# Performance work log

Measured on AMD Instinct MI355X. Metric: run time of the kernel, lower is better.

Reference implementation:

```python
import jax, jax.numpy as jnp
import numpy as np

DOWNSAMPLING_K = 64  # number of pooled key/value positions


def setup_inputs() -> dict:
    key = jax.random.key(0)
    ks = jax.random.split(key, 8)
    B, S, H, N, D = 4, 4096, 1024, 16, 64
    s_in = 0.02  # glorot-like scale for H=1024 fan-in
    return {
        "query": jax.random.normal(ks[0], (B, S, H), jnp.float32),
        "key": jax.random.normal(ks[1], (B, S, H), jnp.float32),
        "value": jax.random.normal(ks[2], (B, S, H), jnp.float32),
        "Wq": jax.random.normal(ks[3], (H, N, D), jnp.float32) * s_in,
        "bq": jnp.zeros((N, D), jnp.float32),
        "Wk": jax.random.normal(ks[4], (H, N, D), jnp.float32) * s_in,
        "bk": jnp.zeros((N, D), jnp.float32),
        "Wv": jax.random.normal(ks[5], (H, N, D), jnp.float32) * s_in,
        "bv": jnp.zeros((N, D), jnp.float32),
        "Wo": jax.random.normal(ks[6], (N, D, H), jnp.float32) * s_in,
        "bo": jnp.zeros((H,), jnp.float32),
        "step": 0,
        "train": 0,
    }


def _downsample(x, k):
    # x: [B, S, N, D] -> mean-pool along sequence into k buckets -> [B, k, N, D]
    B, S, N, D = x.shape
    return x.reshape(B, k, S // k, N, D).mean(axis=2)


def reference(query, key, value, Wq, bq, Wk, bk, Wv, bv, Wo, bo, step, train):
    # QKV projections (DenseGeneral features=(num_heads, head_dim))
    q = jnp.einsum("bsh,hnd->bsnd", query, Wq) + bq  # [B,S,N,D]
    k = jnp.einsum("bsh,hnd->bsnd", key, Wk) + bk
    v = jnp.einsum("bsh,hnd->bsnd", value, Wv) + bv
    # Downsampled (sparse) attention: pool K,V to DOWNSAMPLING_K positions
    kd = _downsample(k, DOWNSAMPLING_K)  # [B,K,N,D]
    vd = _downsample(v, DOWNSAMPLING_K)
    scale = 1.0 / jnp.sqrt(jnp.asarray(q.shape[-1], q.dtype))
    scores = jnp.einsum("bsnd,bknd->bnsk", q, kd) * scale  # [B,N,S,K]
    attn = jax.nn.softmax(scores, axis=-1)
    a_v = jnp.einsum("bnsk,bknd->bsnd", attn, vd)  # [B,S,N,D]
    # Output projection (DenseGeneral over (-2,-1))
    out = jnp.einsum("bsnd,ndh->bsh", a_v, Wo) + bo  # [B,S,H]
    return out
```

## Files before the change

kernel.cpp:

```cpp
#include <hip/hip_runtime.h>

typedef unsigned short u16;
typedef unsigned int u32;
typedef __attribute__((ext_vector_type(8))) short bf16x8_t;
typedef __attribute__((ext_vector_type(4))) float f32x4_t;


#define MFMA_BF16 __builtin_amdgcn_mfma_f32_16x16x32_bf16

__device__ __forceinline__ u16 f2bf(float f) {
  union { float f; u32 u; } a; a.f = f;
  u32 u = a.u;
  u32 r = (u + 0x7FFFu + ((u >> 16) & 1u)) >> 16;
  return (u16)r;
}

__device__ __forceinline__ void async_load16(const void* g, void* l) {
  __builtin_amdgcn_global_load_lds(
      (const __attribute__((address_space(1))) void*)g,
      (__attribute__((address_space(3))) void*)l, 16, 0, 0);
}

__device__ __forceinline__ void stage64(const u16* __restrict__ src,
                                        char* lds_base, int t) {
  const int r = t >> 3;
  const int gch = (t & 7) ^ (r & 7);
  async_load16(src + (size_t)r * 1024 + gch * 8, lds_base + (t >> 6) * 1024);
}

__global__ __launch_bounds__(512) void fused_stream(
    const float* __restrict__ query, const float* __restrict__ key,
    const float* __restrict__ value, const float* __restrict__ W0,
    const float* __restrict__ W1, const float* __restrict__ W2,
    const float* __restrict__ W3, u16* __restrict__ qcvt, u16* __restrict__ keyd,
    u16* __restrict__ valued, u16* __restrict__ T0, u16* __restrict__ T1,
    u16* __restrict__ T2, u16* __restrict__ T3) {
  __shared__ char smem[32768];
  const int z = blockIdx.x;
  const int t = threadIdx.x;
  if (z < 512) {
    f32x4_t (*part)[256] = (f32x4_t(*)[256])smem;
    const int bkk = z & 255;
    const float* x = (z >= 256) ? value : key;
    u16* xd = (z >= 256) ? valued : keyd;
    const int lane = t & 63, w = t >> 6;
    const float* base = x + (size_t)bkk * 65536 + (size_t)w * 8 * 1024;
#define LD4(j, s) \
  __builtin_nontemporal_load((const f32x4_t*)(base + (size_t)(j) * 1024 + ((s) * 64 + lane) * 4))
    f32x4_t a0 = {0.f, 0.f, 0.f, 0.f}, a1 = a0, a2 = a0, a3 = a0;
    f32x4_t u0 = LD4(0, 0), u1 = LD4(0, 1), u2 = LD4(0, 2), u3 = LD4(0, 3);
    f32x4_t u4 = LD4(1, 0), u5 = LD4(1, 1), u6 = LD4(1, 2), u7 = LD4(1, 3);
    f32x4_t v0 = LD4(2, 0), v1 = LD4(2, 1), v2 = LD4(2, 2), v3 = LD4(2, 3);
    f32x4_t v4 = LD4(3, 0), v5 = LD4(3, 1), v6 = LD4(3, 2), v7 = LD4(3, 3);
    a0 += u0; a1 += u1; a2 += u2; a3 += u3;
    a0 += u4; a1 += u5; a2 += u6; a3 += u7;
    u0 = LD4(4, 0); u1 = LD4(4, 1); u2 = LD4(4, 2); u3 = LD4(4, 3);
    u4 = LD4(5, 0); u5 = LD4(5, 1); u6 = LD4(5, 2); u7 = LD4(5, 3);
    a0 += v0; a1 += v1; a2 += v2; a3 += v3;
    a0 += v4; a1 += v5; a2 += v6; a3 += v7;
    v0 = LD4(6, 0); v1 = LD4(6, 1); v2 = LD4(6, 2); v3 = LD4(6, 3);
    v4 = LD4(7, 0); v5 = LD4(7, 1); v6 = LD4(7, 2); v7 = LD4(7, 3);
    a0 += u0; a1 += u1; a2 += u2; a3 += u3;
    a0 += u4; a1 += u5; a2 += u6; a3 += u7;
    a0 += v0; a1 += v1; a2 += v2; a3 += v3;
    a0 += v4; a1 += v5; a2 += v6; a3 += v7;
#undef LD4
    part[w][0 * 64 + lane] = a0;
    part[w][1 * 64 + lane] = a1;
    part[w][2 * 64 + lane] = a2;
    part[w][3 * 64 + lane] = a3;
    __syncthreads();
    if (t < 256) {
      f32x4_t s = {0.f, 0.f, 0.f, 0.f};
#pragma unroll
      for (int w2 = 0; w2 < 8; ++w2) s += part[w2][t];
      ushort4 r;
      r.x = f2bf(s[0] * 0.015625f);
      r.y = f2bf(s[1] * 0.015625f);
      r.z = f2bf(s[2] * 0.015625f);
      r.w = f2bf(s[3] * 0.015625f);
      *(ushort4*)(xd + (size_t)bkk * 1024 + t * 4) = r;
    }
  } else if (z < 4608) {
    const size_t i = ((size_t)(z - 512) * 512 + t) * 8;
    const f32x4_t a = __builtin_nontemporal_load((const f32x4_t*)(query + i));
    const f32x4_t b = __builtin_nontemporal_load((const f32x4_t*)(query + i + 4));
    bf16x8_t o;
    o[0] = (short)f2bf(a[0]); o[1] = (short)f2bf(a[1]);
    o[2] = (short)f2bf(a[2]); o[3] = (short)f2bf(a[3]);
    o[4] = (short)f2bf(b[0]); o[5] = (short)f2bf(b[1]);
    o[6] = (short)f2bf(b[2]); o[7] = (short)f2bf(b[3]);
    *(bf16x8_t*)(qcvt + i) = o;
  } else {
    float (*tile)[65] = (float(*)[65])smem;
    const int blk = z - 4608;
    const int wsel = blk >> 8, tidx = blk & 255;
    const float* W = (wsel == 0) ? W0 : (wsel == 1) ? W1 : (wsel == 2) ? W2 : W3;
    u16* WT = (wsel == 0) ? T0 : (wsel == 1) ? T1 : (wsel == 2) ? T2 : T3;
    const int tr = (tidx >> 4) * 64;
    const int tc = (tidx & 15) * 64;
#pragma unroll
    for (int i = 0; i < 8; ++i) {
      int idx = i * 512 + t;
      int r = idx >> 6, c = idx & 63;
      tile[r][c] = __builtin_nontemporal_load(W + (size_t)(tr + r) * 1024 + tc + c);
    }
    __syncthreads();
#pragma unroll
    for (int i = 0; i < 8; ++i) {
      int idx = i * 512 + t;
      int r = idx >> 6, c = idx & 63;
      WT[(size_t)(tc + r) * 1024 + tr + c] = f2bf(tile[c][r]);
    }
  }
}

__global__ __launch_bounds__(256) void gemm_kv(const u16* __restrict__ A0,
                                               const u16* __restrict__ A1,
                                               const u16* __restrict__ BT0,
                                               const u16* __restrict__ BT1,
                                               const float* __restrict__ bias0,
                                               const float* __restrict__ bias1,
                                               u16* __restrict__ C0,
                                               u16* __restrict__ C1) {
  constexpr int K = 1024, BK = 32;
  __shared__ u16 sA[128 * BK];
  __shared__ u16 sB[128 * BK];
  const int z = blockIdx.z;
  const u16* A = z ? A1 : A0;
  const u16* BT = z ? BT1 : BT0;
  const float* bias = z ? bias1 : bias0;
  u16* Cv = z ? C1 : C0;
  const int t = threadIdx.x;
  const int lane = t & 63;
  const int w = t >> 6;
  const int wr = w >> 1, wc = w & 1;
  const int m0 = blockIdx.x * 128;
  const int n0 = blockIdx.y * 128;
  const int c16 = lane & 15, r16 = lane >> 4;

  f32x4_t acc[4][4] = {};

  for (int k0 = 0; k0 < K; k0 += BK) {
#pragma unroll
    for (int i = 0; i < 2; ++i) {
      const int idx = i * 256 + t;
      const int row = idx >> 2, ch = idx & 3;
      const int gch = ch ^ ((row >> 1) & 3);
      async_load16(A + (size_t)(m0 + row) * K + k0 + gch * 8,
                   (char*)sA + (i * 256 + w * 64) * 16);
    }
#pragma unroll
    for (int i = 0; i < 2; ++i) {
      const int idx = i * 256 + t;
      const int row = idx >> 2, ch = idx & 3;
      const int gch = ch ^ ((row >> 1) & 3);
      async_load16(BT + (size_t)(n0 + row) * K + k0 + gch * 8,
                   (char*)sB + (i * 256 + w * 64) * 16);
    }
    __syncthreads();

    bf16x8_t af[4], bfv[4];
#pragma unroll
    for (int m = 0; m < 4; ++m) {
      const int ra = wr * 64 + m * 16 + c16;
      af[m] = *(const bf16x8_t*)&sA[ra * BK + ((r16 ^ ((ra >> 1) & 3)) << 3)];
    }
#pragma unroll
    for (int n = 0; n < 4; ++n) {
      const int rb = wc * 64 + n * 16 + c16;
      bfv[n] = *(const bf16x8_t*)&sB[rb * BK + ((r16 ^ ((rb >> 1) & 3)) << 3)];
    }
#pragma unroll
    for (int m = 0; m < 4; ++m)
#pragma unroll
      for (int n = 0; n < 4; ++n)
        acc[m][n] = MFMA_BF16(af[m], bfv[n], acc[m][n], 0, 0, 0);
    __syncthreads();
  }

#pragma unroll
  for (int m = 0; m < 4; ++m) {
    const int row0 = m0 + wr * 64 + m * 16 + r16 * 4;
#pragma unroll
    for (int n = 0; n < 4; ++n) {
      const int col = n0 + wc * 64 + n * 16 + c16;
      const float bvl = bias[col];
#pragma unroll
      for (int i = 0; i < 4; ++i) {
        const float val = acc[m][n][i] + bvl;
        if (z)
          Cv[(size_t)col * 256 + row0 + i] = f2bf(val);
        else
          Cv[(size_t)(row0 + i) * 1024 + col] = f2bf(val);
      }
    }
  }
}

#define GEMM256_KLOOP(A_, BT_)                                                          \
  const u16* Ab = (A_) + (size_t)bx * 256 * 1024;                                       \
  const u16* Bb = (BT_) + (size_t)by * 256 * 1024;                                      \
  stage64(Ab,                   lds,                 t);                                \
  stage64(Ab + 128 * 1024,      lds + 128 * 128,     t);                                \
  stage64(Bb,                   lds + 32768,         t);                                \
  stage64(Bb + 64 * 1024,       lds + 32768 + 8192,  t);                                \
  stage64(Bb + 128 * 1024,      lds + 32768 + 16384, t);                                \
  stage64(Bb + 192 * 1024,      lds + 32768 + 24576, t);                                \
  stage64(Ab + 64 * 1024,       lds + 64 * 128,      t);                                \
  stage64(Ab + 192 * 1024,      lds + 192 * 128,     t);                                \
  stage64(Ab + 64,              lds + 65536,         t);                                \
  stage64(Ab + 128 * 1024 + 64, lds + 65536 + 16384, t);                                \
  stage64(Bb + 64,              lds + 98304,         t);                                \
  stage64(Bb + 64 * 1024 + 64,  lds + 98304 + 8192,  t);                                \
  stage64(Bb + 128 * 1024 + 64, lds + 98304 + 16384, t);                                \
  stage64(Bb + 192 * 1024 + 64, lds + 98304 + 24576, t);                                \
  asm volatile("s_waitcnt vmcnt(6)" ::: "memory");                                      \
  __builtin_amdgcn_s_barrier();                                                         \
  for (int kt = 0; kt < 16; ++kt) {                                                     \
    const int slot = kt & 1;                                                            \
    const u16* sAs = (const u16*)(lds + slot * 65536);                                  \
    const u16* sBs = (const u16*)(lds + slot * 65536 + 32768);                          \
    char* sAn = lds + (slot ^ 1) * 65536;                                               \
    char* sAc = lds + slot * 65536;                                                     \
    char* sBc = lds + slot * 65536 + 32768;                                             \
    const int k1 = (kt < 15 ? kt + 1 : 15) * 64;                                        \
    const int k2 = (kt < 14 ? kt + 2 : 15) * 64;                                        \
    bf16x8_t af[4][2];                                                                  \
    _Pragma("unroll") for (int m = 0; m < 4; ++m) {                                     \
      const int row = wm * 128 + m * 16 + c16;                                          \
      _Pragma("unroll") for (int kk = 0; kk < 2; ++kk)                                  \
        af[m][kk] = *(const bf16x8_t*)&sAs[row * 64 + (((kk * 4 + r16) ^ c7) << 3)];    \
    }                                                                                   \
    _Pragma("unroll") for (int n = 0; n < 2; ++n) {                                     \
      const int row = wn * 64 + n * 16 + c16;                                           \
      _Pragma("unroll") for (int kk = 0; kk < 2; ++kk)                                  \
        bfr[n][kk] = *(const bf16x8_t*)&sBs[row * 64 + (((kk * 4 + r16) ^ c7) << 3)];   \
    }                                                                                   \
    stage64(Ab + (size_t)64 * 1024 + k1,  sAn + 64 * 128,  t);                          \
    stage64(Ab + (size_t)192 * 1024 + k1, sAn + 192 * 128, t);                          \
    asm volatile("" ::: "memory");                                                      \
    __builtin_amdgcn_s_barrier();                                                       \
    asm volatile("s_waitcnt lgkmcnt(0)" ::: "memory");                                  \
    __builtin_amdgcn_sched_barrier(0);                                                  \
    __builtin_amdgcn_s_setprio(1);                                                      \
    _Pragma("unroll") for (int m = 0; m < 4; ++m)                                       \
      _Pragma("unroll") for (int n = 0; n < 2; ++n)                                     \
        _Pragma("unroll") for (int kk = 0; kk < 2; ++kk)                                \
          acc[m][n] = MFMA_BF16(af[m][kk], bfr[n][kk], acc[m][n], 0, 0, 0);             \
    __builtin_amdgcn_s_setprio(0);                                                      \
    asm volatile("" ::: "memory");                                                      \
    __builtin_amdgcn_s_barrier();                                                       \
    _Pragma("unroll") for (int n = 2; n < 4; ++n) {                                     \
      const int row = wn * 64 + n * 16 + c16;                                           \
      _Pragma("unroll") for (int kk = 0; kk < 2; ++kk)                                  \
        bfr[n][kk] = *(const bf16x8_t*)&sBs[row * 64 + (((kk * 4 + r16) ^ c7) << 3)];   \
    }                                                                                   \
    stage64(Ab + k2,                      sAc,             t);                          \
    stage64(Ab + (size_t)128 * 1024 + k2, sAc + 128 * 128, t);                          \
    asm volatile("" ::: "memory");                                                      \
    __builtin_amdgcn_s_barrier();                                                       \
    asm volatile("s_waitcnt lgkmcnt(0)" ::: "memory");                                  \
    __builtin_amdgcn_sched_barrier(0);                                                  \
    __builtin_amdgcn_s_setprio(1);                                                      \
    _Pragma("unroll") for (int m = 0; m < 4; ++m)                                       \
      _Pragma("unroll") for (int n = 2; n < 4; ++n)                                     \
        _Pragma("unroll") for (int kk = 0; kk < 2; ++kk)                                \
          acc[m][n] = MFMA_BF16(af[m][kk], bfr[n][kk], acc[m][n], 0, 0, 0);             \
    __builtin_amdgcn_s_setprio(0);                                                      \
    asm volatile("s_waitcnt vmcnt(10)" ::: "memory");                                   \
    __builtin_amdgcn_s_barrier();                                                       \
    _Pragma("unroll") for (int m = 0; m < 4; ++m) {                                     \
      const int row = wm * 128 + 64 + m * 16 + c16;                                     \
      _Pragma("unroll") for (int kk = 0; kk < 2; ++kk)                                  \
        af[m][kk] = *(const bf16x8_t*)&sAs[row * 64 + (((kk * 4 + r16) ^ c7) << 3)];    \
    }                                                                                   \
    stage64(Bb + k2,                     sBc,        t);                                \
    stage64(Bb + (size_t)64 * 1024 + k2, sBc + 8192, t);                                \
    asm volatile("" ::: "memory");                                                      \
    __builtin_amdgcn_s_barrier();                                                       \
    asm volatile("s_waitcnt lgkmcnt(0)" ::: "memory");                                  \
    __builtin_amdgcn_sched_barrier(0);                                                  \
    __builtin_amdgcn_s_setprio(1);                                                      \
    _Pragma("unroll") for (int m = 0; m < 4; ++m)                                       \
      _Pragma("unroll") for (int n = 0; n < 2; ++n)                                     \
        _Pragma("unroll") for (int kk = 0; kk < 2; ++kk)                                \
          acc[4 + m][n] = MFMA_BF16(af[m][kk], bfr[n][kk], acc[4 + m][n], 0, 0, 0);     \
    __builtin_amdgcn_s_setprio(0);                                                      \
    asm volatile("" ::: "memory");                                                      \
    __builtin_amdgcn_s_barrier();                                                       \
    stage64(Bb + (size_t)128 * 1024 + k2, sBc + 16384, t);                              \
    stage64(Bb + (size_t)192 * 1024 + k2, sBc + 24576, t);                              \
    asm volatile("" ::: "memory");                                                      \
    __builtin_amdgcn_s_barrier();                                                       \
    __builtin_amdgcn_sched_barrier(0);                                                  \
    __builtin_amdgcn_s_setprio(1);                                                      \
    _Pragma("unroll") for (int m = 0; m < 4; ++m)                                       \
      _Pragma("unroll") for (int n = 2; n < 4; ++n)                                     \
        _Pragma("unroll") for (int kk = 0; kk < 2; ++kk)                                \
          acc[4 + m][n] = MFMA_BF16(af[m][kk], bfr[n][kk], acc[4 + m][n], 0, 0, 0);     \
    __builtin_amdgcn_s_setprio(0);                                                      \
    asm volatile("s_waitcnt vmcnt(8)" ::: "memory");                                    \
    __builtin_amdgcn_s_barrier();                                                       \
  }

template <bool C_BF16>
__global__ __launch_bounds__(512) void gemm256(const u16* __restrict__ A,
                                               const u16* __restrict__ BT,
                                               const float* __restrict__ bias,
                                               void* __restrict__ Cv) {
  __shared__ u16 sAB[65536];
  char* lds = (char*)sAB;
  const int t = threadIdx.x;
  const int lane = t & 63;
  const int w = t >> 6;
  const int wm = w >> 2, wn = w & 3;
  const int c16 = lane & 15, r16 = lane >> 4, c7 = c16 & 7;
  const int tile = (blockIdx.x & 7) * 32 + (blockIdx.x >> 3);
  const int bx = tile >> 2, by = tile & 3;
  f32x4_t acc[8][4] = {};
  bf16x8_t bfr[4][2];
  GEMM256_KLOOP(A, BT)
#pragma unroll
  for (int m = 0; m < 8; ++m) {
    const int grow = bx * 256 + wm * 128 + m * 16 + r16 * 4;
#pragma unroll
    for (int n = 0; n < 4; ++n) {
      const int col = by * 256 + wn * 64 + n * 16 + c16;
      const float bvl = bias[col];
#pragma unroll
      for (int i = 0; i < 4; ++i) {
        const float val = acc[m][n][i] + bvl;
        if constexpr (C_BF16)
          ((u16*)Cv)[(size_t)(grow + i) * 1024 + col] = f2bf(val);
        else
          ((float*)Cv)[(size_t)(grow + i) * 1024 + col] = val;
      }
    }
  }
}

#define ATTN_EPI_HALF(HALF)                                                              \
  {                                                                                      \
    asm volatile("s_waitcnt lgkmcnt(0)" ::: "memory");                                   \
    _Pragma("unroll") for (int m = 0; m < 4; ++m)                                        \
      _Pragma("unroll") for (int nq = 0; nq < 4; ++nq) {                                 \
        const int d = nq * 16 + c16;                                                     \
        const float bvl = bias[n_head * 64 + d];                                         \
        _Pragma("unroll") for (int i = 0; i < 4; ++i) {                                  \
          const int row = m * 16 + r16 * 4 + i;                                          \
          qh[(row * 128 + ((d * 2) ^ ((row & 7) << 4))) >> 1] =                          \
              f2bf(acc[HALF * 4 + m][nq][i] + bvl);                                      \
        }                                                                                \
      }                                                                                  \
    if (HALF == 0) {                                                                     \
      asm volatile("s_waitcnt vmcnt(0) lgkmcnt(0)" ::: "memory");                        \
      __builtin_amdgcn_s_barrier();                                                      \
    } else {                                                                             \
      asm volatile("s_waitcnt lgkmcnt(0)" ::: "memory");                                 \
    }                                                                                    \
    bf16x8_t aq[4][2];                                                                   \
    _Pragma("unroll") for (int st = 0; st < 4; ++st) {                                   \
      const int row = st * 16 + c16;                                                     \
      const int rsw = (row & 7) << 4;                                                    \
      _Pragma("unroll") for (int dt = 0; dt < 2; ++dt)                                   \
        aq[st][dt] =                                                                     \
            *(const bf16x8_t*)&qh[(row * 128 + ((dt * 64 + r16 * 16) ^ rsw)) >> 1];      \
    }                                                                                    \
    asm volatile("s_waitcnt lgkmcnt(0)" ::: "memory");                                   \
    __builtin_amdgcn_sched_barrier(0);                                                   \
    u16* sP = qh;                                                                        \
    _Pragma("unroll") for (int st = 0; st < 4; ++st) {                                   \
      f32x4_t accs[4];                                                                   \
      _Pragma("unroll") for (int nn = 0; nn < 4; ++nn) {                                 \
        const u16* kr = &kdw[(nn * 16 + c16) * 64];                                      \
        bf16x8_t b0 = *(const bf16x8_t*)&kr[((r16 * 16) ^ swz) >> 1];                    \
        bf16x8_t b1 = *(const bf16x8_t*)&kr[((64 + r16 * 16) ^ swz) >> 1];               \
        f32x4_t a = {0.f, 0.f, 0.f, 0.f};                                                \
        a = MFMA_BF16(aq[st][0], b0, a, 0, 0, 0);                                        \
        a = MFMA_BF16(aq[st][1], b1, a, 0, 0, 0);                                        \
        accs[nn] = a;                                                                    \
      }                                                                                  \
      float ex[4][4], rs[4];                                                             \
      _Pragma("unroll") for (int i = 0; i < 4; ++i) {                                    \
        float mx = fmaxf(fmaxf(accs[0][i], accs[1][i]), fmaxf(accs[2][i], accs[3][i]));  \
        _Pragma("unroll") for (int off = 1; off < 16; off <<= 1)                         \
          mx = fmaxf(mx, __shfl_xor(mx, off));                                           \
        mx *= 0.125f;                                                                    \
        float s = 0.f;                                                                   \
        _Pragma("unroll") for (int nn = 0; nn < 4; ++nn) {                               \
          float e = __expf(accs[nn][i] * 0.125f - mx);                                   \
          ex[nn][i] = e;                                                                 \
          s += e;                                                                        \
        }                                                                                \
        _Pragma("unroll") for (int off = 1; off < 16; off <<= 1)                         \
          s += __shfl_xor(s, off);                                                       \
        rs[i] = 1.f / s;                                                                 \
      }                                                                                  \
      _Pragma("unroll") for (int i = 0; i < 4; ++i) {                                    \
        const int row = r16 * 4 + i;                                                     \
        const int rsw = (row & 7) << 4;                                                  \
        _Pragma("unroll") for (int nn = 0; nn < 4; ++nn)                                 \
          sP[row * 64 + (((nn * 32 + c16 * 2) ^ rsw) >> 1)] = f2bf(ex[nn][i]);           \
      }                                                                                  \
      asm volatile("s_waitcnt lgkmcnt(0)" ::: "memory");                                 \
      bf16x8_t pa0 = *(const bf16x8_t*)&sP[c16 * 64 + (((r16 * 16) ^ swz) >> 1)];        \
      bf16x8_t pa1 = *(const bf16x8_t*)&sP[c16 * 64 + (((64 + r16 * 16) ^ swz) >> 1)];   \
      f32x4_t accv[4];                                                                   \
      _Pragma("unroll") for (int dt = 0; dt < 4; ++dt) {                                 \
        const u16* vr = &vdw[(dt * 16 + c16) * 64];                                      \
        bf16x8_t v0 = *(const bf16x8_t*)&vr[((r16 * 16) ^ swz) >> 1];                    \
        bf16x8_t v1 = *(const bf16x8_t*)&vr[((64 + r16 * 16) ^ swz) >> 1];               \
        f32x4_t a = {0.f, 0.f, 0.f, 0.f};                                                \
        a = MFMA_BF16(pa0, v0, a, 0, 0, 0);                                              \
        a = MFMA_BF16(pa1, v1, a, 0, 0, 0);                                              \
        accv[dt] = a;                                                                    \
      }                                                                                  \
      _Pragma("unroll") for (int i = 0; i < 4; ++i) {                                    \
        const int row = r16 * 4 + i;                                                     \
        const int rsw = (row & 7) << 4;                                                  \
        _Pragma("unroll") for (int dt = 0; dt < 4; ++dt)                                 \
          sP[row * 64 + (((dt * 32 + c16 * 2) ^ rsw) >> 1)] = f2bf(accv[dt][i] * rs[i]); \
      }                                                                                  \
      asm volatile("s_waitcnt lgkmcnt(0)" ::: "memory");                                 \
      const int srow_base = b * 4096 + s0b + wm * 128 + HALF * 64 + st * 16;             \
      _Pragma("unroll") for (int r = 0; r < 2; ++r) {                                    \
        const int row = r * 8 + (lane >> 3);                                             \
        const int cb = ((lane & 7) * 16) ^ ((row & 7) << 4);                             \
        bf16x8_t vv = *(const bf16x8_t*)&sP[row * 64 + (cb >> 1)];                       \
        *(bf16x8_t*)(av + (size_t)(srow_base + row) * 1024 + n_head * 64 +               \
                     (lane & 7) * 8) = vv;                                               \
      }                                                                                  \
    }                                                                                    \
  }

__global__ __launch_bounds__(512) void gemm256_attn(const u16* __restrict__ A,
                                                    const u16* __restrict__ BT,
                                                    const float* __restrict__ bias,
                                                    const u16* __restrict__ kdb,
                                                    const u16* __restrict__ vdTb,
                                                    u16* __restrict__ av) {
  __shared__ u16 sAB[65536];
  char* lds = (char*)sAB;
  const int t = threadIdx.x;
  const int lane = t & 63;
  const int w = t >> 6;
  const int wm = w >> 2, wn = w & 3;
  const int c16 = lane & 15, r16 = lane >> 4, c7 = c16 & 7;
  const int tile = (blockIdx.x & 7) * 32 + (blockIdx.x >> 3);
  const int bx = tile >> 2, by = tile & 3;
  f32x4_t acc[8][4] = {};
  bf16x8_t bfr[4][2];
  GEMM256_KLOOP(A, BT)

  asm volatile("s_waitcnt vmcnt(0)" ::: "memory");
  __builtin_amdgcn_s_barrier();

  const int b = bx >> 4;
  const int s0b = (bx & 15) * 256;
  char* kdL = lds + 65536;
  char* vdL = lds + 65536 + 32768;
  {
    const int kk = t >> 3;
    const int colb = ((t & 7) ^ (kk & 7)) << 4;
#pragma unroll
    for (int h = 0; h < 4; ++h) {
      const int n = by * 4 + h;
      async_load16((const char*)kdb + (size_t)(b * 64 + kk) * 2048 + n * 128 + colb,
                   kdL + h * 8192 + (t >> 6) * 1024);
      async_load16((const char*)vdTb + (size_t)(n * 64 + kk) * 512 + b * 128 + colb,
                   vdL + h * 8192 + (t >> 6) * 1024);
    }
  }
  u16* qh = (u16*)(lds + w * 8192);
  const int n_head = by * 4 + wn;
  const u16* kdw = (const u16*)(kdL + wn * 8192);
  const u16* vdw = (const u16*)(vdL + wn * 8192);
  const int swz = (c16 & 7) << 4;

  ATTN_EPI_HALF(0)
  ATTN_EPI_HALF(1)
}

extern "C" void kernel_launch(void* const* d_in, const int* in_sizes, int n_in,
                              void* d_out, int out_size, void* d_ws, size_t ws_size,
                              hipStream_t stream) {
  (void)in_sizes; (void)n_in; (void)out_size; (void)ws_size;
  const float* query = (const float*)d_in[0];
  const float* key   = (const float*)d_in[1];
  const float* value = (const float*)d_in[2];
  const float* Wq = (const float*)d_in[3];
  const float* bq = (const float*)d_in[4];
  const float* Wk = (const float*)d_in[5];
  const float* bk = (const float*)d_in[6];
  const float* Wv = (const float*)d_in[7];
  const float* bv = (const float*)d_in[8];
  const float* Wo = (const float*)d_in[9];
  const float* bo = (const float*)d_in[10];
  float* out = (float*)d_out;

  char* ws = (char*)d_ws;
  const size_t MB = 1024 * 1024;
  u16* WqT    = (u16*)(ws + 0 * MB);
  u16* WkT    = (u16*)(ws + 2 * MB);
  u16* WvT    = (u16*)(ws + 4 * MB);
  u16* WoT    = (u16*)(ws + 6 * MB);
  u16* keyd   = (u16*)(ws + 8 * MB);
  u16* valued = (u16*)(ws + 8 * MB + 512 * 1024);
  u16* kdb    = (u16*)(ws + 9 * MB);
  u16* vdTb   = (u16*)(ws + 9 * MB + 512 * 1024);
  u16* avb    = (u16*)(ws + 10 * MB);
  u16* qcvt   = (u16*)((char*)d_out + 32 * MB);

  fused_stream<<<5632, 512, 0, stream>>>(query, key, value, Wq, Wk, Wv, Wo,
                                         qcvt, keyd, valued, WqT, WkT, WvT, WoT);

  gemm_kv<<<dim3(2, 8, 2), 256, 0, stream>>>(keyd, valued, WkT, WvT, bk, bv, kdb, vdTb);

  gemm256_attn<<<256, 512, 0, stream>>>(qcvt, WqT, bq, kdb, vdTb, avb);
  gemm256<false><<<256, 512, 0, stream>>>(avb, WoT, bo, out);
}
```

Baseline: 157.6 us.

## Replace 256x256 output-projection GEMM with a 128x128-tile kernel on more blocks

The final output projection (attention output times Wo, fp32 result) now uses a new gemm128 kernel instead of gemm256. It uses 128x128 tiles, 256 threads, 4 waves in a 2x2 layout and a double-buffered 64 KB LDS ring. Blocks are remapped across XCDs, and the grid grows from 256 to 1024 blocks. The aim is better load balance and latency hiding, since several smaller blocks can share a CU. The trade-off is lower per-block data reuse and more global reads of the A and B operands.

```diff
diff --git a/kernel.cpp b/kernel.cpp
--- a/kernel.cpp
+++ b/kernel.cpp
@@ -22,6 +22,13 @@
 }
 
 __device__ __forceinline__ void stage64(const u16* __restrict__ src,
+                                        char* lds_base, int t) {
+  const int r = t >> 3;
+  const int gch = (t & 7) ^ (r & 7);
+  async_load16(src + (size_t)r * 1024 + gch * 8, lds_base + (t >> 6) * 1024);
+}
+
+__device__ __forceinline__ void stage32(const u16* __restrict__ src,
                                         char* lds_base, int t) {
   const int r = t >> 3;
   const int gch = (t & 7) ^ (r & 7);
@@ -304,38 +311,161 @@
     __builtin_amdgcn_s_barrier();                                                       \
   }
 
-template <bool C_BF16>
-__global__ __launch_bounds__(512) void gemm256(const u16* __restrict__ A,
+__global__ __launch_bounds__(256) void gemm128(const u16* __restrict__ A,
                                                const u16* __restrict__ BT,
                                                const float* __restrict__ bias,
-                                               void* __restrict__ Cv) {
-  __shared__ u16 sAB[65536];
+                                               float* __restrict__ Cv) {
+  __shared__ u16 sAB[32768];
   char* lds = (char*)sAB;
   const int t = threadIdx.x;
   const int lane = t & 63;
   const int w = t >> 6;
-  const int wm = w >> 2, wn = w & 3;
+  const int wm = w >> 1, wn = w & 1;
   const int c16 = lane & 15, r16 = lane >> 4, c7 = c16 & 7;
-  const int tile = (blockIdx.x & 7) * 32 + (blockIdx.x >> 3);
-  const int bx = tile >> 2, by = tile & 3;
-  f32x4_t acc[8][4] = {};
+  const int lin = blockIdx.x;
+  const int xcd = lin & 7, c = lin >> 3;
+  const int bx = xcd * 16 + (c >> 3);
+  const int by = c & 7;
+  const u16* Ab = A + (size_t)bx * 128 * 1024;
+  const u16* Bb = BT + (size_t)by * 128 * 1024;
+
+  f32x4_t acc[4][4] = {};
   bf16x8_t bfr[4][2];
-  GEMM256_KLOOP(A, BT)
-#pragma unroll
-  for (int m = 0; m < 8; ++m) {
-    const int grow = bx * 256 + wm * 128 + m * 16 + r16 * 4;
+
+  stage32(Ab,                  lds,                 t);
+  stage32(Ab + 64 * 1024,      lds + 8192,          t);
+  stage32(Bb,                  lds + 16384,         t);
+  stage32(Bb + 32 * 1024,      lds + 16384 + 4096,  t);
+  stage32(Bb + 64 * 1024,      lds + 16384 + 8192,  t);
+  stage32(Bb + 96 * 1024,      lds + 16384 + 12288, t);
+  stage32(Ab + 32 * 1024,      lds + 4096,          t);
+  stage32(Ab + 96 * 1024,      lds + 12288,         t);
+  stage32(Ab + 64,             lds + 32768,         t);
+  stage32(Ab + 64 * 1024 + 64, lds + 32768 + 8192,  t);
+  stage32(Bb + 64,             lds + 49152,         t);
+  stage32(Bb + 32 * 1024 + 64, lds + 49152 + 4096,  t);
+  stage32(Bb + 64 * 1024 + 64, lds + 49152 + 8192,  t);
+  stage32(Bb + 96 * 1024 + 64, lds + 49152 + 12288, t);
+  asm volatile("s_waitcnt vmcnt(6)" ::: "memory");
+  __builtin_amdgcn_s_barrier();
+
+  for (int kt = 0; kt < 16; ++kt) {
+    const int slot = kt & 1;
+    const u16* sAs = (const u16*)(lds + slot * 32768);
+    const u16* sBs = (const u16*)(lds + slot * 32768 + 16384);
+    char* sAn = lds + (slot ^ 1) * 32768;
+    char* sAc = lds + slot * 32768;
+    char* sBc = lds + slot * 32768 + 16384;
+    const int k1 = (kt < 15 ? kt + 1 : 15) * 64;
+    const int k2 = (kt < 14 ? kt + 2 : 15) * 64;
+    bf16x8_t af[4][2];
+#pragma unroll
+    for (int m = 0; m < 2; ++m) {
+      const int row = wm * 64 + m * 16 + c16;
+#pragma unroll
+      for (int kk = 0; kk < 2; ++kk)
+        af[m][kk] = *(const bf16x8_t*)&sAs[row * 64 + (((kk * 4 + r16) ^ c7) << 3)];
+    }
+#pragma unroll
+    for (int n = 0; n < 2; ++n) {
+      const int row = wn * 64 + n * 16 + c16;
+#pragma unroll
+      for (int kk = 0; kk < 2; ++kk)
+        bfr[n][kk] = *(const bf16x8_t*)&sBs[row * 64 + (((kk * 4 + r16) ^ c7) << 3)];
+    }
+    stage32(Ab + (size_t)32 * 1024 + k1, sAn + 4096,  t);
+    stage32(Ab + (size_t)96 * 1024 + k1, sAn + 12288, t);
+    asm volatile("" ::: "memory");
+    __builtin_amdgcn_s_barrier();
+    asm volatile("s_waitcnt lgkmcnt(0)" ::: "memory");
+    __builtin_amdgcn_sched_barrier(0);
+    __builtin_amdgcn_s_setprio(1);
+#pragma unroll
+    for (int m = 0; m < 2; ++m)
+#pragma unroll
+      for (int n = 0; n < 2; ++n)
+#pragma unroll
+        for (int kk = 0; kk < 2; ++kk)
+          acc[m][n] = MFMA_BF16(af[m][kk], bfr[n][kk], acc[m][n], 0, 0, 0);
+    __builtin_amdgcn_s_setprio(0);
+    asm volatile("" ::: "memory");
+    __builtin_amdgcn_s_barrier();
+#pragma unroll
+    for (int n = 2; n < 4; ++n) {
+      const int row = wn * 64 + n * 16 + c16;
+#pragma unroll
+      for (int kk = 0; kk < 2; ++kk)
+        bfr[n][kk] = *(const bf16x8_t*)&sBs[row * 64 + (((kk * 4 + r16) ^ c7) << 3)];
+    }
+    stage32(Ab + k2,                     sAc,        t);
+    stage32(Ab + (size_t)64 * 1024 + k2, sAc + 8192, t);
+    asm volatile("" ::: "memory");
+    __builtin_amdgcn_s_barrier();
+    asm volatile("s_waitcnt lgkmcnt(0)" ::: "memory");
+    __builtin_amdgcn_sched_barrier(0);
+    __builtin_amdgcn_s_setprio(1);
+#pragma unroll
+    for (int m = 0; m < 2; ++m)
+#pragma unroll
+      for (int n = 2; n < 4; ++n)
+#pragma unroll
+        for (int kk = 0; kk < 2; ++kk)
+          acc[m][n] = MFMA_BF16(af[m][kk], bfr[n][kk], acc[m][n], 0, 0, 0);
+    __builtin_amdgcn_s_setprio(0);
+    asm volatile("s_waitcnt vmcnt(10)" ::: "memory");
+    __builtin_amdgcn_s_barrier();
+#pragma unroll
+    for (int m = 0; m < 2; ++m) {
+      const int row = wm * 64 + 32 + m * 16 + c16;
+#pragma unroll
+      for (int kk = 0; kk < 2; ++kk)
+        af[m][kk] = *(const bf16x8_t*)&sAs[row * 64 + (((kk * 4 + r16) ^ c7) << 3)];
+    }
+    stage32(Bb + k2,                     sBc,        t);
+    stage32(Bb + (size_t)32 * 1024 + k2, sBc + 4096, t);
+    asm volatile("" ::: "memory");
+    __builtin_amdgcn_s_barrier();
+    asm volatile("s_waitcnt lgkmcnt(0)" ::: "memory");
+    __builtin_amdgcn_sched_barrier(0);
+    __builtin_amdgcn_s_setprio(1);
+#pragma unroll
+    for (int m = 0; m < 2; ++m)
+#pragma unroll
+      for (int n = 0; n < 2; ++n)
+#pragma unroll
+        for (int kk = 0; kk < 2; ++kk)
+          acc[2 + m][n] = MFMA_BF16(af[m][kk], bfr[n][kk], acc[2 + m][n], 0, 0, 0);
+    __builtin_amdgcn_s_setprio(0);
+    asm volatile("" ::: "memory");
+    __builtin_amdgcn_s_barrier();
+    stage32(Bb + (size_t)64 * 1024 + k2, sBc + 8192,  t);
+    stage32(Bb + (size_t)96 * 1024 + k2, sBc + 12288, t);
+    asm volatile("" ::: "memory");
+    __builtin_amdgcn_s_barrier();
+    __builtin_amdgcn_sched_barrier(0);
+    __builtin_amdgcn_s_setprio(1);
+#pragma unroll
+    for (int m = 0; m < 2; ++m)
+#pragma unroll
+      for (int n = 2; n < 4; ++n)
+#pragma unroll
+        for (int kk = 0; kk < 2; ++kk)
+          acc[2 + m][n] = MFMA_BF16(af[m][kk], bfr[n][kk], acc[2 + m][n], 0, 0, 0);
+    __builtin_amdgcn_s_setprio(0);
+    asm volatile("s_waitcnt vmcnt(8)" ::: "memory");
+    __builtin_amdgcn_s_barrier();
+  }
+
+#pragma unroll
+  for (int m = 0; m < 4; ++m) {
+    const int grow = bx * 128 + wm * 64 + m * 16 + r16 * 4;
 #pragma unroll
     for (int n = 0; n < 4; ++n) {
-      const int col = by * 256 + wn * 64 + n * 16 + c16;
+      const int col = by * 128 + wn * 64 + n * 16 + c16;
       const float bvl = bias[col];
 #pragma unroll
-      for (int i = 0; i < 4; ++i) {
-        const float val = acc[m][n][i] + bvl;
-        if constexpr (C_BF16)
-          ((u16*)Cv)[(size_t)(grow + i) * 1024 + col] = f2bf(val);
-        else
-          ((float*)Cv)[(size_t)(grow + i) * 1024 + col] = val;
-      }
+      for (int i = 0; i < 4; ++i)
+        Cv[(size_t)(grow + i) * 1024 + col] = acc[m][n][i] + bvl;
     }
   }
 }
@@ -518,5 +648,5 @@
   gemm_kv<<<dim3(2, 8, 2), 256, 0, stream>>>(keyd, valued, WkT, WvT, bk, bv, kdb, vdTb);
 
   gemm256_attn<<<256, 512, 0, stream>>>(qcvt, WqT, bq, kdb, vdTb, avb);
-  gemm256<false><<<256, 512, 0, stream>>>(avb, WoT, bo, out);
-}
+  gemm128<<<1024, 256, 0, stream>>>(avb, WoT, bo, out);
+}
```

Result: slower. 164.1 us (+4.1%).
